# Kernel optimization log

Measured on AMD Instinct MI355X. Metric: run time of the kernel, lower is better.

The kernel has to match this reference:

```python
import jax, jax.numpy as jnp
import numpy as np

V = 32000; D = 128; L = 2048; B = 4
DI = 256; DS = 16; K = 4; H = 4; NM = 6; NA = 2; PAD = 0


def setup_inputs() -> dict:
    key = jax.random.key(0)
    ks = jax.random.split(key, 24)
    n = lambda i, shape, s: jax.random.normal(ks[i], shape, dtype=jnp.float32) * s
    inp = {}
    inp["input_ids"] = jax.random.randint(ks[0], (B, L), 0, V)
    inp["token_types"] = jax.random.randint(ks[1], (B, L), 0, 10)
    inp["timestamps"] = jax.random.uniform(ks[2], (B, L), dtype=jnp.float32)
    inp["emb"] = n(3, (V, D), 0.02).at[PAD].set(0.0)
    inp["type_emb"] = n(4, (10, D), 0.02)
    inp["te_freqs"] = n(5, (D // 2,), 0.1)
    inp["te_phases"] = jnp.zeros((D // 2,), jnp.float32)
    inp["te_w"] = n(6, (D, D), 0.05)
    inp["te_b"] = jnp.zeros((D,), jnp.float32)
    # Mamba blocks (stacked over NM)
    inp["m_norm_w"] = jnp.ones((NM, D), jnp.float32)
    inp["m_norm_b"] = jnp.zeros((NM, D), jnp.float32)
    inp["m_in_w"] = n(7, (NM, 2 * DI, D), 0.05)
    inp["m_conv_w"] = n(8, (NM, DI, 1, K), 0.2)   # depthwise, OIH with I=1
    inp["m_conv_b"] = jnp.zeros((NM, DI), jnp.float32)
    inp["m_dt_w"] = n(9, (NM, DI, DI), 0.05)
    inp["m_dt_b"] = jnp.zeros((NM, DI), jnp.float32)
    inp["m_B_w"] = n(10, (NM, DS, DI), 0.05)
    inp["m_C_w"] = n(11, (NM, DS, DI), 0.05)
    inp["m_D"] = jnp.ones((NM, DI), jnp.float32)
    inp["m_A_log"] = jnp.broadcast_to(jnp.log(jnp.arange(1, DS + 1, dtype=jnp.float32)), (NM, DI, DS)) + 0.0
    inp["m_out_w"] = n(12, (NM, D, DI), 0.05)
    # Attention blocks (stacked over NA)
    inp["a_ln1_w"] = jnp.ones((NA, D), jnp.float32)
    inp["a_ln1_b"] = jnp.zeros((NA, D), jnp.float32)
    inp["a_qkv_w"] = n(13, (NA, 3 * D, D), 0.05)
    inp["a_qkv_b"] = jnp.zeros((NA, 3 * D), jnp.float32)
    inp["a_out_w"] = n(14, (NA, D, D), 0.05)
    inp["a_out_b"] = jnp.zeros((NA, D), jnp.float32)
    inp["a_ln2_w"] = jnp.ones((NA, D), jnp.float32)
    inp["a_ln2_b"] = jnp.zeros((NA, D), jnp.float32)
    inp["a_f1_w"] = n(15, (NA, 4 * D, D), 0.05)
    inp["a_f1_b"] = jnp.zeros((NA, 4 * D), jnp.float32)
    inp["a_f2_w"] = n(16, (NA, D, 4 * D), 0.05)
    inp["a_f2_b"] = jnp.zeros((NA, D), jnp.float32)
    # Task head (n_tasks=1)
    inp["h_ln_w"] = jnp.ones((D,), jnp.float32)
    inp["h_ln_b"] = jnp.zeros((D,), jnp.float32)
    inp["h_w"] = n(17, (1, D), 0.05)
    inp["h_b"] = jnp.zeros((1,), jnp.float32)
    return inp


def _ln(x, w, b, eps=1e-5):
    mu = x.mean(-1, keepdims=True)
    var = ((x - mu) ** 2).mean(-1, keepdims=True)
    return (x - mu) * jax.lax.rsqrt(var + eps) * w + b


def _mamba(x, nw, nb, inw, cw, cb, dtw, dtb, bw, cpw, Dp, Alog, ow):
    res = x
    xn = _ln(x, nw, nb)
    xz = xn @ inw.T                              # [B,L,2*DI]
    xp, z = jnp.split(xz, 2, axis=-1)
    # causal depthwise conv: left-pad K-1, take first L outputs
    xc = jax.lax.conv_general_dilated(
        xp.transpose(0, 2, 1), cw, (1,), [(K - 1, 0)],
        feature_group_count=DI, dimension_numbers=("NCH", "OIH", "NCH"))
    xc = (xc + cb[None, :, None]).transpose(0, 2, 1)
    xc = jax.nn.silu(xc)
    dt = jax.nn.softplus(xc @ dtw.T + dtb)       # [B,L,DI]
    Bm = xc @ bw.T                               # [B,L,DS]
    Cm = xc @ cpw.T                              # [B,L,DS]
    A = -jnp.exp(Alog)                           # [DI,DS]

    def step(h, inp):
        dt_t, x_t, b_t, c_t = inp                # [B,DI],[B,DI],[B,DS],[B,DS]
        h = h * jnp.exp(A * dt_t[..., None]) + (x_t * dt_t)[..., None] * b_t[:, None, :]
        return h, (h * c_t[:, None, :]).sum(-1)

    xs = (jnp.moveaxis(dt, 1, 0), jnp.moveaxis(xc, 1, 0),
          jnp.moveaxis(Bm, 1, 0), jnp.moveaxis(Cm, 1, 0))
    h0 = jnp.zeros((x.shape[0], DI, DS), x.dtype)
    _, y = jax.lax.scan(step, h0, xs)            # y: [L,B,DI]
    y = jnp.moveaxis(y, 0, 1)
    y = y + xc * Dp
    y = y * jax.nn.silu(z)
    return res + y @ ow.T


def _attn(x, l1w, l1b, qkvw, qkvb, ow, ob, l2w, l2b, f1w, f1b, f2w, f2b):
    res = x
    xn = _ln(x, l1w, l1b)
    qkv = xn @ qkvw.T + qkvb
    q, k, v = jnp.split(qkv, 3, axis=-1)
    dh = D // H
    rs = lambda t: t.reshape(t.shape[0], t.shape[1], H, dh)
    q, k, v = rs(q), rs(k), rs(v)
    sc = jnp.einsum("bqhd,bkhd->bhqk", q, k) / jnp.sqrt(jnp.float32(dh))
    p = jax.nn.softmax(sc, axis=-1)
    o = jnp.einsum("bhqk,bkhd->bqhd", p, v).reshape(x.shape)
    x = res + o @ ow.T + ob
    ff = jax.nn.gelu(_ln(x, l2w, l2b) @ f1w.T + f1b, approximate=False) @ f2w.T + f2b
    return x + ff


def reference(input_ids, token_types, timestamps, emb, type_emb, te_freqs, te_phases, te_w, te_b,
              m_norm_w, m_norm_b, m_in_w, m_conv_w, m_conv_b, m_dt_w, m_dt_b, m_B_w, m_C_w,
              m_D, m_A_log, m_out_w,
              a_ln1_w, a_ln1_b, a_qkv_w, a_qkv_b, a_out_w, a_out_b, a_ln2_w, a_ln2_b,
              a_f1_w, a_f1_b, a_f2_w, a_f2_b, h_ln_w, h_ln_b, h_w, h_b):
    t = timestamps[..., None]
    enc = jnp.concatenate([jnp.sin(t * te_freqs + te_phases),
                           jnp.cos(t * te_freqs + te_phases)], axis=-1)
    x = emb[input_ids] + type_emb[token_types] + enc @ te_w.T + te_b
    attn_every = (NM + NA) // NA
    mi = 0; ai = 0
    for i in range(NM + NA):
        if (i + 1) % attn_every == 0:
            x = _attn(x, a_ln1_w[ai], a_ln1_b[ai], a_qkv_w[ai], a_qkv_b[ai],
                      a_out_w[ai], a_out_b[ai], a_ln2_w[ai], a_ln2_b[ai],
                      a_f1_w[ai], a_f1_b[ai], a_f2_w[ai], a_f2_b[ai])
            ai += 1
        else:
            x = _mamba(x, m_norm_w[mi], m_norm_b[mi], m_in_w[mi], m_conv_w[mi], m_conv_b[mi],
                       m_dt_w[mi], m_dt_b[mi], m_B_w[mi], m_C_w[mi], m_D[mi], m_A_log[mi], m_out_w[mi])
            mi += 1
    cls = x[:, 0, :]
    return (_ln(cls, h_ln_w, h_ln_b) @ h_w.T + h_b)[:, 0]
```

## Files before the change

kernel.cpp:

```cpp
#include <hip/hip_runtime.h>
#include <hip/hip_bf16.h>
#include <math.h>

constexpr int Ll = 2048, Bb = 4, DIi = 256, Hh = 4;
constexpr int TOK = Bb * Ll;
constexpr int NC = 128;
constexpr int CH = 16;
constexpr float LOG2E = 1.442695040888963f;

#define DEV __device__ __forceinline__

DEV float siluf(float v)     { return v / (1.f + expf(-v)); }
DEV float softplusf(float v) { return (v > 20.f) ? v : log1pf(expf(v)); }
DEV float geluf(float v)     { return 0.5f * v * (1.f + erff(v * 0.7071067811865476f)); }

#if defined(__has_builtin)
#if __has_builtin(__builtin_amdgcn_exp2f)
#define EXP2F __builtin_amdgcn_exp2f
#endif
#endif
#ifndef EXP2F
#define EXP2F exp2f
#endif

DEV short f2bf(float f) {
    union { float f; unsigned u; } a; a.f = f;
    unsigned r = (a.u + 0x7fffu + ((a.u >> 16) & 1u)) >> 16;
    return (short)r;
}

using bf16x8 = __attribute__((ext_vector_type(8))) short;
using f16x8  = __attribute__((ext_vector_type(8))) _Float16;
using f32x4  = __attribute__((ext_vector_type(4))) float;

__global__ __launch_bounds__(256) void wprep_kernel(
    const float* s0, const float* s1, const float* s2, const float* s3,
    const float* s4, const float* s5, const float* s6, const float* s7,
    const float* s8, const float* s9, _Float16* dst)
{
    constexpr int base[10] = {0, 16384, 409600, 802816, 827392, 851968,
                              1048576, 1146880, 1179648, 1310720};
    constexpr int nseg[10] = {16384, 393216, 393216, 24576, 24576, 196608,
                              98304, 32768, 131072, 131072};
    int seg = blockIdx.y;
    int t = blockIdx.x * 256 + threadIdx.x;
    if (t >= nseg[seg]) return;
    const float* src;
    switch (seg) {
        case 0: src = s0; break; case 1: src = s1; break;
        case 2: src = s2; break; case 3: src = s3; break;
        case 4: src = s4; break; case 5: src = s5; break;
        case 6: src = s6; break; case 7: src = s7; break;
        case 8: src = s8; break; default: src = s9; break;
    }
    dst[base[seg] + t] = (_Float16)src[t];
}

__global__ __launch_bounds__(256) void gather_enc_kernel(
    const int* __restrict__ ids, const int* __restrict__ tts,
    const float* __restrict__ ts, const float* __restrict__ emb,
    const float* __restrict__ temb, const float* __restrict__ freqs,
    const float* __restrict__ phases, float* __restrict__ x,
    float* __restrict__ enc)
{
    int tok = blockIdx.x * 2 + (threadIdx.x >> 7);
    int d = threadIdx.x & 127;
    float tval = ts[tok];
    int j = d & 63;
    float a = tval * freqs[j] + phases[j];
    enc[(size_t)tok * 128 + d] = (d < 64) ? sinf(a) : cosf(a);
    int id = ids[tok];
    int tt = tts[tok];
    x[(size_t)tok * 128 + d] = emb[(size_t)id * 128 + d] + temb[(size_t)tt * 128 + d];
}

template <int ACT, bool BIAS, bool ADD, bool LNA, int MODE>
__global__ __launch_bounds__(256) void gemm64_kernel(
    const float* __restrict__ A, const _Float16* __restrict__ W,
    const float* __restrict__ bias, float* __restrict__ C,
    const float* __restrict__ lnw, const float* __restrict__ lnb,
    const _Float16* __restrict__ Bw, const _Float16* __restrict__ Cw,
    float* __restrict__ bmo, float* __restrict__ cmo,
    short* __restrict__ kbf, short* __restrict__ vbf,
    int M, int N, int Kd, int lda, int ldc)
{
    constexpr int PADK = LNA ? 136 : 72;
    __shared__ _Float16 As[64][PADK];
    __shared__ _Float16 Ws[64][PADK];
    __shared__ float sMu[LNA ? 64 : 1];
    __shared__ float sRs[LNA ? 64 : 1];
    const int by = blockIdx.y;
    const bool isBC = (MODE == 1) && (by == (int)gridDim.y - 1);
    const int bm0 = blockIdx.x * 64, bn0 = by * 64;
    const int tid = threadIdx.x;
    const int w = tid >> 6, l = tid & 63;
    const int wr = w >> 1, wc = w & 1;
    const int fr = l & 15, fk = (l >> 4) * 8;
    const int srow = tid >> 2;
    f32x4 acc[2][2] = {};

    if (LNA) {
        const int kofs = (tid & 3) * 32;
        const float* ap = A + (size_t)(bm0 + srow) * lda + kofs;
        float av[32];
#pragma unroll
        for (int q = 0; q < 8; q++)
            *(float4*)(av + q * 4) = *(const float4*)(ap + q * 4);
        float s = 0.f, sq = 0.f;
#pragma unroll
        for (int q = 0; q < 32; q++) { s += av[q]; sq += av[q] * av[q]; }
        s  += __shfl_xor(s, 1);  s  += __shfl_xor(s, 2);
        sq += __shfl_xor(sq, 1); sq += __shfl_xor(sq, 2);
        if ((tid & 3) == 0) {
            float mu = s * (1.f / 128.f);
            float var = sq * (1.f / 128.f) - mu * mu;
            sMu[srow] = mu;
            sRs[srow] = rsqrtf(var + 1e-5f);
        }
        const _Float16* wp = W + (size_t)(bn0 + srow) * Kd + kofs;
        f16x8 wv0 = *(const f16x8*)wp,        wv1 = *(const f16x8*)(wp + 8);
        f16x8 wv2 = *(const f16x8*)(wp + 16), wv3 = *(const f16x8*)(wp + 24);
        __syncthreads();
        float mu = sMu[srow], rs = sRs[srow];
#pragma unroll
        for (int v = 0; v < 4; v++) {
            f16x8 a16;
#pragma unroll
            for (int j = 0; j < 8; j++) {
                float g = lnw[kofs + v * 8 + j];
                float bb = lnb[kofs + v * 8 + j];
                a16[j] = (_Float16)((av[v * 8 + j] - mu) * rs * g + bb);
            }
            *(f16x8*)&As[srow][kofs + v * 8] = a16;
        }
        *(f16x8*)&Ws[srow][kofs]      = wv0;
        *(f16x8*)&Ws[srow][kofs + 8]  = wv1;
        *(f16x8*)&Ws[srow][kofs + 16] = wv2;
        *(f16x8*)&Ws[srow][kofs + 24] = wv3;
        __syncthreads();
#pragma unroll
        for (int ks = 0; ks < 128; ks += 32) {
            f16x8 afr0 = *(const f16x8*)&As[wr * 32 + fr][ks + fk];
            f16x8 afr1 = *(const f16x8*)&As[wr * 32 + 16 + fr][ks + fk];
            f16x8 wfr0 = *(const f16x8*)&Ws[wc * 32 + fr][ks + fk];
            f16x8 wfr1 = *(const f16x8*)&Ws[wc * 32 + 16 + fr][ks + fk];
            acc[0][0] = __builtin_amdgcn_mfma_f32_16x16x32_f16(afr0, wfr0, acc[0][0], 0, 0, 0);
            acc[0][1] = __builtin_amdgcn_mfma_f32_16x16x32_f16(afr0, wfr1, acc[0][1], 0, 0, 0);
            acc[1][0] = __builtin_amdgcn_mfma_f32_16x16x32_f16(afr1, wfr0, acc[1][0], 0, 0, 0);
            acc[1][1] = __builtin_amdgcn_mfma_f32_16x16x32_f16(afr1, wfr1, acc[1][1], 0, 0, 0);
        }
    } else {
        const int skc = (tid & 3) * 16;
        for (int k0 = 0; k0 < Kd; k0 += 64) {
            const float* ap = A + (size_t)(bm0 + srow) * lda + k0 + skc;
            const _Float16* wp;
            if (isBC) {
                if (srow < 16)      wp = Bw + (size_t)srow * Kd + k0 + skc;
                else if (srow < 32) wp = Cw + (size_t)(srow - 16) * Kd + k0 + skc;
                else                wp = Bw + k0 + skc;
            } else {
                wp = W + (size_t)(bn0 + srow) * Kd + k0 + skc;
            }
            float af[16];
#pragma unroll
            for (int q = 0; q < 4; q++)
                *(float4*)(af + q * 4) = *(const float4*)(ap + q * 4);
            f16x8 wb0 = *(const f16x8*)wp;
            f16x8 wb1 = *(const f16x8*)(wp + 8);
            f16x8 ab0, ab1;
#pragma unroll
            for (int q = 0; q < 8; q++) {
                ab0[q] = (_Float16)af[q]; ab1[q] = (_Float16)af[q + 8];
            }
            __syncthreads();
            *(f16x8*)&As[srow][skc]     = ab0;
            *(f16x8*)&As[srow][skc + 8] = ab1;
            *(f16x8*)&Ws[srow][skc]     = wb0;
            *(f16x8*)&Ws[srow][skc + 8] = wb1;
            __syncthreads();
#pragma unroll
            for (int ks = 0; ks < 64; ks += 32) {
                f16x8 afr0 = *(const f16x8*)&As[wr * 32 + fr][ks + fk];
                f16x8 afr1 = *(const f16x8*)&As[wr * 32 + 16 + fr][ks + fk];
                f16x8 wfr0 = *(const f16x8*)&Ws[wc * 32 + fr][ks + fk];
                f16x8 wfr1 = *(const f16x8*)&Ws[wc * 32 + 16 + fr][ks + fk];
                acc[0][0] = __builtin_amdgcn_mfma_f32_16x16x32_f16(afr0, wfr0, acc[0][0], 0, 0, 0);
                acc[0][1] = __builtin_amdgcn_mfma_f32_16x16x32_f16(afr0, wfr1, acc[0][1], 0, 0, 0);
                acc[1][0] = __builtin_amdgcn_mfma_f32_16x16x32_f16(afr1, wfr0, acc[1][0], 0, 0, 0);
                acc[1][1] = __builtin_amdgcn_mfma_f32_16x16x32_f16(afr1, wfr1, acc[1][1], 0, 0, 0);
            }
        }
    }
#pragma unroll
    for (int ri = 0; ri < 2; ri++)
#pragma unroll
    for (int ci = 0; ci < 2; ci++) {
        const int lcol = wc * 32 + ci * 16 + fr;
        const int col = bn0 + lcol;
        const int row0 = bm0 + wr * 32 + ri * 16 + (l >> 4) * 4;
        if (isBC) {
            if (lcol < 32) {
                float* dst = (lcol < 16) ? bmo : cmo;
                const int cc = lcol & 15;
#pragma unroll
                for (int r = 0; r < 4; r++)
                    dst[(size_t)(row0 + r) * 16 + cc] = acc[ri][ci][r];
            }
        } else if (MODE == 2) {
            const float bv = bias[col];
            const int b = row0 >> 11, tl0 = row0 & 2047;
            if (col < 128) {
#pragma unroll
                for (int r = 0; r < 4; r++)
                    C[(size_t)(row0 + r) * 128 + col] = acc[ri][ci][r] + bv;
            } else if (col < 256) {
                const int hc = col - 128;
                short* kp = kbf + ((size_t)(b * 4 + (hc >> 5)) * 2048 + tl0) * 32 + (hc & 31);
#pragma unroll
                for (int r = 0; r < 4; r++)
                    kp[(size_t)r * 32] = f2bf(acc[ri][ci][r] + bv);
            } else {
                const int hc = col - 256;
                short4 vk;
#pragma unroll
                for (int r = 0; r < 4; r++)
                    ((short*)&vk)[r] = f2bf(acc[ri][ci][r] + bv);
                *(short4*)(vbf + ((size_t)(b * 4 + (hc >> 5)) * 32 + (hc & 31)) * 2048 + tl0) = vk;
            }
        } else {
            const float bv = BIAS ? bias[col] : 0.f;
#pragma unroll
            for (int r = 0; r < 4; r++) {
                float t = acc[ri][ci][r] + bv;
                if (ACT == 1) t = softplusf(t);
                if (ACT == 2) t = geluf(t);
                float* p = C + (size_t)(row0 + r) * ldc + col;
                if (ADD) t += *p;
                *p = t;
            }
        }
    }
}

__global__ __launch_bounds__(256) void conv_kernel(
    const float* __restrict__ xz, const float* __restrict__ cw,
    const float* __restrict__ cb, float* __restrict__ xc)
{
    int g = blockIdx.x * 256 + threadIdx.x;
    int c4 = g & 63;
    int t  = (g >> 6) & 2047;
    int b  = g >> 17;
    int c  = c4 * 4;
    float4 w0 = *(const float4*)(cw + (size_t)c * 4);
    float4 w1 = *(const float4*)(cw + (size_t)(c + 1) * 4);
    float4 w2 = *(const float4*)(cw + (size_t)(c + 2) * 4);
    float4 w3 = *(const float4*)(cw + (size_t)(c + 3) * 4);
    float4 bi = *(const float4*)(cb + c);
    float4 xk[4];
#pragma unroll
    for (int kk = 0; kk < 4; kk++) {
        int tt = t - 3 + kk;
        if (tt >= 0) xk[kk] = *(const float4*)(xz + ((size_t)b * 2048 + tt) * 512 + c);
        else xk[kk] = make_float4(0.f, 0.f, 0.f, 0.f);
    }
    float4 r;
    r.x = bi.x + xk[0].x * w0.x + xk[1].x * w0.y + xk[2].x * w0.z + xk[3].x * w0.w;
    r.y = bi.y + xk[0].y * w1.x + xk[1].y * w1.y + xk[2].y * w1.z + xk[3].y * w1.w;
    r.z = bi.z + xk[0].z * w2.x + xk[1].z * w2.y + xk[2].z * w2.z + xk[3].z * w2.w;
    r.w = bi.w + xk[0].w * w3.x + xk[1].w * w3.y + xk[2].w * w3.z + xk[3].w * w3.w;
    r.x = siluf(r.x); r.y = siluf(r.y); r.z = siluf(r.z); r.w = siluf(r.w);
    *(float4*)(xc + ((size_t)b * 2048 + t) * 256 + c) = r;
}

__global__ __launch_bounds__(256) void scan1_kernel(
    const float* __restrict__ dt, const float* __restrict__ xc,
    const float* __restrict__ bm, const float* __restrict__ Alog,
    float* __restrict__ F, float* __restrict__ sumdt)
{
    int c = threadIdx.x;
    int k = blockIdx.x & (NC - 1);
    int b = blockIdx.x / NC;
    __shared__ float sB[CH][16];
    int t0 = k * CH;
    if (threadIdx.x < CH * 4) {
        int r = threadIdx.x >> 2, c4 = (threadIdx.x & 3) << 2;
        *(float4*)&sB[r][c4] = *(const float4*)(bm + ((size_t)b * 2048 + t0 + r) * 16 + c4);
    }
    float A2[16];
#pragma unroll
    for (int s = 0; s < 16; s++) A2[s] = -expf(Alog[(size_t)c * 16 + s]) * LOG2E;
    __syncthreads();
    float h[16] = {};
    float sd = 0.f;
    size_t base = ((size_t)b * 2048 + t0) * 256 + c;
    for (int tt = 0; tt < CH; tt++) {
        float d  = dt[base + (size_t)tt * 256];
        float xv = xc[base + (size_t)tt * 256];
        sd += d;
        float xdt = xv * d;
#pragma unroll
        for (int s = 0; s < 16; s++) h[s] = h[s] * EXP2F(A2[s] * d) + xdt * sB[tt][s];
    }
    size_t fo = (((size_t)b * NC + k) * 256 + c) * 16;
#pragma unroll
    for (int s = 0; s < 16; s += 4) *(float4*)(F + fo + s) = make_float4(h[s], h[s+1], h[s+2], h[s+3]);
    sumdt[((size_t)b * NC + k) * 256 + c] = sd;
}

__global__ __launch_bounds__(256) void scan2_kernel(
    float* __restrict__ F, const float* __restrict__ sumdt,
    const float* __restrict__ Alog)
{
    int g = blockIdx.x * 256 + threadIdx.x;
    int s = g & 15, c = (g >> 4) & 255, b = g >> 12;
    float A2 = -expf(Alog[(size_t)c * 16 + s]) * LOG2E;
    float h = 0.f;
    for (int k = 0; k < NC; k++) {
        size_t o = (((size_t)b * NC + k) * 256 + c) * 16 + s;
        float tmp = F[o];
        F[o] = h;
        h = h * EXP2F(A2 * sumdt[((size_t)b * NC + k) * 256 + c]) + tmp;
    }
}

__global__ __launch_bounds__(256) void scan3_kernel(
    const float* __restrict__ dt, const float* __restrict__ xc,
    const float* __restrict__ bm, const float* __restrict__ cm,
    const float* __restrict__ xz, const float* __restrict__ Alog,
    const float* __restrict__ Dp, const float* __restrict__ Hs,
    float* __restrict__ y)
{
    int c = threadIdx.x;
    int k = blockIdx.x & (NC - 1);
    int b = blockIdx.x / NC;
    __shared__ float sB[CH][16], sC[CH][16];
    int t0 = k * CH;
    if (threadIdx.x < CH * 4) {
        int r = threadIdx.x >> 2, c4 = (threadIdx.x & 3) << 2;
        *(float4*)&sB[r][c4] = *(const float4*)(bm + ((size_t)b * 2048 + t0 + r) * 16 + c4);
        *(float4*)&sC[r][c4] = *(const float4*)(cm + ((size_t)b * 2048 + t0 + r) * 16 + c4);
    }
    float A2[16];
#pragma unroll
    for (int s = 0; s < 16; s++) A2[s] = -expf(Alog[(size_t)c * 16 + s]) * LOG2E;
    __syncthreads();
    float h[16];
    size_t ho = (((size_t)b * NC + k) * 256 + c) * 16;
#pragma unroll
    for (int s = 0; s < 16; s++) h[s] = Hs[ho + s];
    float Dv = Dp[c];
    size_t base  = ((size_t)b * 2048 + t0) * 256 + c;
    size_t zbase = ((size_t)b * 2048 + t0) * 512 + 256 + c;
    for (int tt = 0; tt < CH; tt++) {
        float d  = dt[base + (size_t)tt * 256];
        float xv = xc[base + (size_t)tt * 256];
        float xdt = xv * d;
        float yv = 0.f;
#pragma unroll
        for (int s = 0; s < 16; s++) {
            h[s] = h[s] * EXP2F(A2[s] * d) + xdt * sB[tt][s];
            yv += h[s] * sC[tt][s];
        }
        yv += xv * Dv;
        float zv = xz[zbase + (size_t)tt * 512];
        y[base + (size_t)tt * 256] = yv * siluf(zv);
    }
}

__global__ __launch_bounds__(256) void attn_part_kernel(
    const float* __restrict__ qbuf, const short* __restrict__ kbf,
    const short* __restrict__ vbf, float* __restrict__ pO, float* __restrict__ pml)
{
    __shared__ short Klds[2][64 * 32];
    __shared__ short Vlds[2][32 * 64];
    __shared__ short Pt[4][64][18];
    const int qt = blockIdx.x, b = blockIdx.z;
    const int h = blockIdx.y >> 2, sp = blockIdx.y & 3;
    const int tid = threadIdx.x;
    const int w = tid >> 6, l = tid & 63;
    const int q16 = l & 15, g = l >> 4;
    const float cQ = 0.25503634043f;

    const int qrow = qt * 64 + w * 16 + q16;
    const float* qp = qbuf + ((size_t)(b * 2048 + qrow)) * 128 + 32 * h + g * 8;
    bf16x8 qfrag;
    {
        float qf[8];
        *(float4*)qf       = *(const float4*)qp;
        *(float4*)(qf + 4) = *(const float4*)(qp + 4);
#pragma unroll
        for (int i = 0; i < 8; i++) qfrag[i] = f2bf(qf[i] * cQ);
    }
    const int bh = b * 4 + h;
    const short* kb = kbf + ((size_t)bh * 2048) * 32;
    const short* vb = vbf + ((size_t)bh * 32) * 2048;

    const int vrow = tid >> 3;
    const int vsw  = ((tid & 7) * 16) ^ ((vrow & 7) << 4);
    const int ts0 = sp * 8;

    bf16x8 kst, vst;
    auto ldregs = [&](int t) {
        kst = *(const bf16x8*)(kb + (size_t)t * 2048 + tid * 8);
        vst = *(const bf16x8*)(vb + (size_t)vrow * 2048 + t * 64 + (vsw >> 1));
    };
    auto dswrite = [&](int buf) {
        *(bf16x8*)&Klds[buf][tid * 8] = kst;
        *(bf16x8*)&Vlds[buf][tid * 8] = vst;
    };

    float m = -1e30f, lsum = 0.f;
    f32x4 O0 = {0.f, 0.f, 0.f, 0.f}, O1 = {0.f, 0.f, 0.f, 0.f};
    const f32x4 zf = {0.f, 0.f, 0.f, 0.f};

    auto step = [&](int buf) {
        bf16x8 kf[4];
#pragma unroll
        for (int kt = 0; kt < 4; kt++)
            kf[kt] = *(const bf16x8*)&Klds[buf][(kt * 16 + q16) * 32 + g * 8];
        f32x4 St[4];
#pragma unroll
        for (int kt = 0; kt < 4; kt++)
            St[kt] = __builtin_amdgcn_mfma_f32_16x16x32_bf16(kf[kt], qfrag, zf, 0, 0, 0);
        float pm = St[0][0];
#pragma unroll
        for (int kt = 0; kt < 4; kt++)
#pragma unroll
            for (int r = 0; r < 4; r++) pm = fmaxf(pm, St[kt][r]);
        pm = fmaxf(pm, __shfl_xor(pm, 16));
        pm = fmaxf(pm, __shfl_xor(pm, 32));
        float mn = fmaxf(m, pm);
        float rs = EXP2F(m - mn);
        float ps = 0.f;
#pragma unroll
        for (int kt = 0; kt < 4; kt++)
#pragma unroll
            for (int r = 0; r < 4; r++) {
                float p = EXP2F(St[kt][r] - mn);
                ps += p;
                Pt[w][kt * 16 + g * 4 + r][q16] = f2bf(p);
            }
        ps += __shfl_xor(ps, 16);
        ps += __shfl_xor(ps, 32);
        lsum = lsum * rs + ps;
        m = mn;
        O0 *= rs; O1 *= rs;
#pragma unroll
        for (int c = 0; c < 2; c++) {
            bf16x8 pb;
#pragma unroll
            for (int i = 0; i < 8; i++) pb[i] = Pt[w][c * 32 + g * 8 + i][q16];
#pragma unroll
            for (int hf = 0; hf < 2; hf++) {
                const int d = q16 + 16 * hf;
                bf16x8 vf = *(const bf16x8*)&Vlds[buf][d * 64 + ((c * 32 + g * 8) ^ ((d & 7) << 3))];
                if (hf == 0) O0 = __builtin_amdgcn_mfma_f32_16x16x32_bf16(vf, pb, O0, 0, 0, 0);
                else         O1 = __builtin_amdgcn_mfma_f32_16x16x32_bf16(vf, pb, O1, 0, 0, 0);
            }
        }
    };

    ldregs(ts0);
    dswrite(0);
    ldregs(ts0 + 1);
    int cur = 0;
    for (int i = 0; i < 8; i++) {
        __syncthreads();
        if (i + 1 < 8) {
            dswrite(cur ^ 1);
            if (i + 2 < 8) ldregs(ts0 + i + 2);
        }
        step(cur);
        cur ^= 1;
    }

    size_t po = (((size_t)(bh * 4 + sp)) * 2048 + qrow) * 32;
#pragma unroll
    for (int r = 0; r < 4; r++) {
        pO[po + g * 4 + r]      = O0[r];
        pO[po + 16 + g * 4 + r] = O1[r];
    }
    if (g == 0) {
        size_t mo = (((size_t)(bh * 4 + sp)) * 2048 + qrow) * 2;
        pml[mo]     = m;
        pml[mo + 1] = lsum;
    }
}

__global__ __launch_bounds__(256) void attn_comb_kernel(
    const float* __restrict__ pO, const float* __restrict__ pml,
    float* __restrict__ aout)
{
    int gid = blockIdx.x * 256 + threadIdx.x;
    int d = gid & 31, q = (gid >> 5) & 2047, bh = gid >> 16;
    float m[4], lv[4], M = -1e30f;
#pragma unroll
    for (int s = 0; s < 4; s++) {
        size_t mo = (((size_t)(bh * 4 + s)) * 2048 + q) * 2;
        m[s] = pml[mo]; lv[s] = pml[mo + 1];
        M = fmaxf(M, m[s]);
    }
    float L = 0.f, o = 0.f;
#pragma unroll
    for (int s = 0; s < 4; s++) {
        float wgt = EXP2F(m[s] - M);
        L += lv[s] * wgt;
        o += pO[(((size_t)(bh * 4 + s)) * 2048 + q) * 32 + d] * wgt;
    }
    int b = bh >> 2, h = bh & 3;
    aout[((size_t)(b * 2048 + q)) * 128 + h * 32 + d] = o / L;
}

__global__ __launch_bounds__(128) void head_kernel(
    const float* __restrict__ x, const float* __restrict__ w,
    const float* __restrict__ bsp, const float* __restrict__ hw,
    const float* __restrict__ hb, float* __restrict__ out)
{
    int bb = blockIdx.x;
    int d = threadIdx.x;
    int wid = d >> 6, lane = d & 63;
    float v = x[(size_t)bb * 2048 * 128 + d];
    float s = v, sq = v * v;
#pragma unroll
    for (int o = 32; o > 0; o >>= 1) { s += __shfl_xor(s, o); sq += __shfl_xor(sq, o); }
    __shared__ float red[4];
    if (lane == 0) { red[wid] = s; red[2 + wid] = sq; }
    __syncthreads();
    s = red[0] + red[1]; sq = red[2] + red[3];
    float mu = s * (1.f / 128.f);
    float var = sq * (1.f / 128.f) - mu * mu;
    float xn = (v - mu) * rsqrtf(var + 1e-5f) * w[d] + bsp[d];
    float pr = xn * hw[d];
#pragma unroll
    for (int o = 32; o > 0; o >>= 1) pr += __shfl_xor(pr, o);
    __syncthreads();
    if (lane == 0) red[wid] = pr;
    __syncthreads();
    if (d == 0) out[bb] = red[0] + red[1] + hb[0];
}

constexpr size_t OFF_X  = 0;
constexpr size_t OFF_XZ = (size_t)1 << 20;
constexpr size_t OFF_XC = (size_t)5 << 20;
constexpr size_t OFF_DT = (size_t)7 << 20;
constexpr size_t OFF_Y  = (size_t)9 << 20;
constexpr size_t OFF_BM = (size_t)11 << 20;
constexpr size_t OFF_CM = OFF_BM + 131072;
constexpr size_t OFF_SD = OFF_CM + 131072;
constexpr size_t OFF_ST = OFF_SD + 131072;
constexpr size_t OFF_F  = OFF_ST + 16384;
constexpr size_t OFF_WF = OFF_F + ((size_t)2 << 20);
constexpr size_t WS_FLOATS = OFF_WF + 720896;

extern "C" void kernel_launch(void* const* d_in, const int* in_sizes, int n_in,
                              void* d_out, int out_size, void* d_ws, size_t ws_size,
                              hipStream_t stream)
{
    const int*   ids   = (const int*)d_in[0];
    const int*   tts   = (const int*)d_in[1];
    const float* tstmp = (const float*)d_in[2];
    const float* emb   = (const float*)d_in[3];
    const float* temb  = (const float*)d_in[4];
    const float* tef   = (const float*)d_in[5];
    const float* tep   = (const float*)d_in[6];
    const float* tew   = (const float*)d_in[7];
    const float* tebi  = (const float*)d_in[8];
    const float* mnw   = (const float*)d_in[9];
    const float* mnb   = (const float*)d_in[10];
    const float* minw  = (const float*)d_in[11];
    const float* mcwp  = (const float*)d_in[12];
    const float* mcb   = (const float*)d_in[13];
    const float* mdtw  = (const float*)d_in[14];
    const float* mdtb  = (const float*)d_in[15];
    const float* mbw   = (const float*)d_in[16];
    const float* mcw2  = (const float*)d_in[17];
    const float* mD    = (const float*)d_in[18];
    const float* mAl   = (const float*)d_in[19];
    const float* mow   = (const float*)d_in[20];
    const float* al1w  = (const float*)d_in[21];
    const float* al1b  = (const float*)d_in[22];
    const float* aqkvw = (const float*)d_in[23];
    const float* aqkvb = (const float*)d_in[24];
    const float* aow   = (const float*)d_in[25];
    const float* aob   = (const float*)d_in[26];
    const float* al2w  = (const float*)d_in[27];
    const float* al2b  = (const float*)d_in[28];
    const float* af1w  = (const float*)d_in[29];
    const float* af1b  = (const float*)d_in[30];
    const float* af2w  = (const float*)d_in[31];
    const float* af2b  = (const float*)d_in[32];
    const float* hlnw  = (const float*)d_in[33];
    const float* hlnb  = (const float*)d_in[34];
    const float* hw    = (const float*)d_in[35];
    const float* hb    = (const float*)d_in[36];
    float* out = (float*)d_out;
    float* wsf = (float*)d_ws;
    if (ws_size < WS_FLOATS * sizeof(float)) return;

    float* x    = wsf + OFF_X;
    float* xz   = wsf + OFF_XZ;
    float* xc   = wsf + OFF_XC;
    float* dtb  = wsf + OFF_DT;
    float* yb   = wsf + OFF_Y;
    float* bm   = wsf + OFF_BM;
    float* cm   = wsf + OFF_CM;
    float* sdb  = wsf + OFF_SD;
    float* Fb   = wsf + OFF_F;
    float* ff   = xz;
    float* aout = yb;
    float* qbuf = xc;
    float* pO   = xz;
    float* pml  = dtb;
    float* encb = Fb;
    short* kbf  = (short*)(wsf + OFF_F);
    short* vbf  = (short*)(wsf + OFF_F + ((size_t)1 << 20));
    _Float16* wf16 = (_Float16*)(wsf + OFF_WF);

    const _Float16* tew16   = wf16;
    const _Float16* minw16  = wf16 + 16384;
    const _Float16* mdtw16  = wf16 + 409600;
    const _Float16* mbw16   = wf16 + 802816;
    const _Float16* mcw216  = wf16 + 827392;
    const _Float16* mow16   = wf16 + 851968;
    const _Float16* aqkvw16 = wf16 + 1048576;
    const _Float16* aow16   = wf16 + 1146880;
    const _Float16* af1w16  = wf16 + 1179648;
    const _Float16* af2w16  = wf16 + 1310720;

    wprep_kernel<<<dim3(1536, 10), 256, 0, stream>>>(
        tew, minw, mdtw, mbw, mcw2, mow, aqkvw, aow, af1w, af2w, wf16);

    gather_enc_kernel<<<TOK / 2, 256, 0, stream>>>(ids, tts, tstmp, emb, temb, tef, tep, x, encb);
    gemm64_kernel<0, true, true, false, 0><<<dim3(128, 2), 256, 0, stream>>>(
        encb, tew16, tebi, x, nullptr, nullptr, nullptr, nullptr,
        nullptr, nullptr, nullptr, nullptr, TOK, 128, 128, 128, 128);

    int mi = 0, ai = 0;
    for (int i = 0; i < 8; i++) {
        if ((i + 1) % 4 == 0) {
            gemm64_kernel<0, true, false, true, 2><<<dim3(128, 6), 256, 0, stream>>>(
                x, aqkvw16 + (size_t)ai * 49152, aqkvb + ai * 384, qbuf,
                al1w + ai * 128, al1b + ai * 128, nullptr, nullptr,
                nullptr, nullptr, kbf, vbf, TOK, 384, 128, 128, 128);
            attn_part_kernel<<<dim3(32, 16, Bb), 256, 0, stream>>>(qbuf, kbf, vbf, pO, pml);
            attn_comb_kernel<<<4096, 256, 0, stream>>>(pO, pml, aout);
            gemm64_kernel<0, true, true, false, 0><<<dim3(128, 2), 256, 0, stream>>>(
                aout, aow16 + (size_t)ai * 16384, aob + ai * 128, x,
                nullptr, nullptr, nullptr, nullptr,
                nullptr, nullptr, nullptr, nullptr, TOK, 128, 128, 128, 128);
            gemm64_kernel<2, true, false, true, 0><<<dim3(128, 8), 256, 0, stream>>>(
                x, af1w16 + (size_t)ai * 65536, af1b + ai * 512, ff,
                al2w + ai * 128, al2b + ai * 128, nullptr, nullptr,
                nullptr, nullptr, nullptr, nullptr, TOK, 512, 128, 128, 512);
            gemm64_kernel<0, true, true, false, 0><<<dim3(128, 2), 256, 0, stream>>>(
                ff, af2w16 + (size_t)ai * 65536, af2b + ai * 128, x,
                nullptr, nullptr, nullptr, nullptr,
                nullptr, nullptr, nullptr, nullptr, TOK, 128, 512, 512, 128);
            ai++;
        } else {
            const float* Al = mAl + (size_t)mi * DIi * 16;
            gemm64_kernel<0, false, false, true, 0><<<dim3(128, 8), 256, 0, stream>>>(
                x, minw16 + (size_t)mi * 65536, nullptr, xz,
                mnw + mi * 128, mnb + mi * 128, nullptr, nullptr,
                nullptr, nullptr, nullptr, nullptr, TOK, 512, 128, 128, 512);
            conv_kernel<<<2048, 256, 0, stream>>>(xz, mcwp + (size_t)mi * DIi * 4, mcb + mi * DIi, xc);
            gemm64_kernel<1, true, false, false, 1><<<dim3(128, 5), 256, 0, stream>>>(
                xc, mdtw16 + (size_t)mi * 65536, mdtb + mi * 256, dtb,
                nullptr, nullptr,
                mbw16 + (size_t)mi * 4096, mcw216 + (size_t)mi * 4096,
                bm, cm, nullptr, nullptr, TOK, 256, 256, 256, 256);
            scan1_kernel<<<Bb * NC, 256, 0, stream>>>(dtb, xc, bm, Al, Fb, sdb);
            scan2_kernel<<<64, 256, 0, stream>>>(Fb, sdb, Al);
            scan3_kernel<<<Bb * NC, 256, 0, stream>>>(dtb, xc, bm, cm, xz, Al, mD + mi * 256, Fb, yb);
            gemm64_kernel<0, false, true, false, 0><<<dim3(128, 2), 256, 0, stream>>>(
                yb, mow16 + (size_t)mi * 32768, nullptr, x,
                nullptr, nullptr, nullptr, nullptr,
                nullptr, nullptr, nullptr, nullptr, TOK, 128, 256, 256, 128);
            mi++;
        }
    }
    head_kernel<<<Bb, 128, 0, stream>>>(x, hlnw, hlnb, hw, hb, out);
}
```

Measured before the change: 714.1 us.

## Fuse depthwise conv into dt GEMM and attention combine into out-proj GEMM

The causal depthwise conv + SiLU is now computed inside the dt/B/C GEMM's A-tile load, with blocks in the first column tile also writing xc for the scan, so the standalone conv kernel is dropped. The attention split-softmax combine is folded into the out-projection GEMM's A-load (new MODE 3), removing attn_comb_kernel and the aout round-trip. scan1 is also restructured to load dt and x*dt for the chunk first and then run the recurrence per state, which exposes more independent work. The cost is redundant conv and combine work across column-tile blocks and extra global loads per A tile.

```diff
diff --git a/kernel.cpp b/kernel.cpp
--- a/kernel.cpp
+++ b/kernel.cpp
@@ -82,6 +82,9 @@
     const _Float16* __restrict__ Bw, const _Float16* __restrict__ Cw,
     float* __restrict__ bmo, float* __restrict__ cmo,
     short* __restrict__ kbf, short* __restrict__ vbf,
+    const float* __restrict__ cvw, const float* __restrict__ cvb,
+    float* __restrict__ xco,
+    const float* __restrict__ pOin, const float* __restrict__ pmlin,
     int M, int N, int Kd, int lda, int ldc)
 {
     constexpr int PADK = LNA ? 136 : 72;
@@ -89,6 +92,8 @@
     __shared__ _Float16 Ws[64][PADK];
     __shared__ float sMu[LNA ? 64 : 1];
     __shared__ float sRs[LNA ? 64 : 1];
+    __shared__ float cwS[(MODE == 1) ? 256 : 1][4];
+    __shared__ float cbS[(MODE == 1) ? 256 : 1];
     const int by = blockIdx.y;
     const bool isBC = (MODE == 1) && (by == (int)gridDim.y - 1);
     const int bm0 = blockIdx.x * 64, bn0 = by * 64;
@@ -99,6 +104,12 @@
     const int srow = tid >> 2;
     f32x4 acc[2][2] = {};
 
+    if (MODE == 1) {
+        *(float4*)&cwS[tid][0] = *(const float4*)(cvw + (size_t)tid * 4);
+        cbS[tid] = cvb[tid];
+        __syncthreads();
+    }
+
     if (LNA) {
         const int kofs = (tid & 3) * 32;
         const float* ap = A + (size_t)(bm0 + srow) * lda + kofs;
@@ -152,7 +163,75 @@
     } else {
         const int skc = (tid & 3) * 16;
         for (int k0 = 0; k0 < Kd; k0 += 64) {
-            const float* ap = A + (size_t)(bm0 + srow) * lda + k0 + skc;
+            float af[16];
+            if (MODE == 1) {
+                const int tglob = bm0 + srow;
+                const int bb = tglob >> 11, tl = tglob & 2047;
+                const size_t rowb = (size_t)bb * 2048;
+#pragma unroll
+                for (int q4 = 0; q4 < 4; q4++) {
+                    const int cb0 = k0 + skc + q4 * 4;
+                    float4 xr[4];
+#pragma unroll
+                    for (int kk = 0; kk < 4; kk++) {
+                        int tt = tl - 3 + kk;
+                        xr[kk] = (tt >= 0) ? *(const float4*)(A + (rowb + tt) * 512 + cb0)
+                                           : make_float4(0.f, 0.f, 0.f, 0.f);
+                    }
+#pragma unroll
+                    for (int j = 0; j < 4; j++) {
+                        const int col = cb0 + j;
+                        float a0 = cbS[col]
+                            + ((const float*)&xr[0])[j] * cwS[col][0]
+                            + ((const float*)&xr[1])[j] * cwS[col][1]
+                            + ((const float*)&xr[2])[j] * cwS[col][2]
+                            + ((const float*)&xr[3])[j] * cwS[col][3];
+                        af[q4 * 4 + j] = siluf(a0);
+                    }
+                }
+                if (by == 0) {
+#pragma unroll
+                    for (int q4 = 0; q4 < 4; q4++)
+                        *(float4*)(xco + (size_t)tglob * 256 + k0 + skc + q4 * 4) =
+                            make_float4(af[q4*4], af[q4*4+1], af[q4*4+2], af[q4*4+3]);
+                }
+            } else if (MODE == 3) {
+                const int tglob = bm0 + srow;
+                const int bb = tglob >> 11, q = tglob & 2047;
+                const int base = k0 + skc;
+                const int h = base >> 5, d0 = base & 31;
+                const int bh = bb * 4 + h;
+                float m[4], lv[4], M = -1e30f;
+#pragma unroll
+                for (int s = 0; s < 4; s++) {
+                    size_t mo = (((size_t)(bh * 4 + s)) * 2048 + q) * 2;
+                    m[s] = pmlin[mo]; lv[s] = pmlin[mo + 1];
+                    M = fmaxf(M, m[s]);
+                }
+                float L = 0.f, wgt[4];
+#pragma unroll
+                for (int s = 0; s < 4; s++) { wgt[s] = EXP2F(m[s] - M); L += lv[s] * wgt[s]; }
+                float inv = 1.f / L;
+#pragma unroll
+                for (int j = 0; j < 16; j++) af[j] = 0.f;
+#pragma unroll
+                for (int s = 0; s < 4; s++) {
+                    const float* pp = pOin + (((size_t)(bh * 4 + s)) * 2048 + q) * 32 + d0;
+#pragma unroll
+                    for (int q4 = 0; q4 < 4; q4++) {
+                        float4 v = *(const float4*)(pp + q4 * 4);
+                        af[q4*4+0] += v.x * wgt[s]; af[q4*4+1] += v.y * wgt[s];
+                        af[q4*4+2] += v.z * wgt[s]; af[q4*4+3] += v.w * wgt[s];
+                    }
+                }
+#pragma unroll
+                for (int j = 0; j < 16; j++) af[j] *= inv;
+            } else {
+                const float* ap = A + (size_t)(bm0 + srow) * lda + k0 + skc;
+#pragma unroll
+                for (int q = 0; q < 4; q++)
+                    *(float4*)(af + q * 4) = *(const float4*)(ap + q * 4);
+            }
             const _Float16* wp;
             if (isBC) {
                 if (srow < 16)      wp = Bw + (size_t)srow * Kd + k0 + skc;
@@ -161,10 +240,6 @@
             } else {
                 wp = W + (size_t)(bn0 + srow) * Kd + k0 + skc;
             }
-            float af[16];
-#pragma unroll
-            for (int q = 0; q < 4; q++)
-                *(float4*)(af + q * 4) = *(const float4*)(ap + q * 4);
             f16x8 wb0 = *(const f16x8*)wp;
             f16x8 wb1 = *(const f16x8*)(wp + 8);
             f16x8 ab0, ab1;
@@ -242,36 +317,6 @@
     }
 }
 
-__global__ __launch_bounds__(256) void conv_kernel(
-    const float* __restrict__ xz, const float* __restrict__ cw,
-    const float* __restrict__ cb, float* __restrict__ xc)
-{
-    int g = blockIdx.x * 256 + threadIdx.x;
-    int c4 = g & 63;
-    int t  = (g >> 6) & 2047;
-    int b  = g >> 17;
-    int c  = c4 * 4;
-    float4 w0 = *(const float4*)(cw + (size_t)c * 4);
-    float4 w1 = *(const float4*)(cw + (size_t)(c + 1) * 4);
-    float4 w2 = *(const float4*)(cw + (size_t)(c + 2) * 4);
-    float4 w3 = *(const float4*)(cw + (size_t)(c + 3) * 4);
-    float4 bi = *(const float4*)(cb + c);
-    float4 xk[4];
-#pragma unroll
-    for (int kk = 0; kk < 4; kk++) {
-        int tt = t - 3 + kk;
-        if (tt >= 0) xk[kk] = *(const float4*)(xz + ((size_t)b * 2048 + tt) * 512 + c);
-        else xk[kk] = make_float4(0.f, 0.f, 0.f, 0.f);
-    }
-    float4 r;
-    r.x = bi.x + xk[0].x * w0.x + xk[1].x * w0.y + xk[2].x * w0.z + xk[3].x * w0.w;
-    r.y = bi.y + xk[0].y * w1.x + xk[1].y * w1.y + xk[2].y * w1.z + xk[3].y * w1.w;
-    r.z = bi.z + xk[0].z * w2.x + xk[1].z * w2.y + xk[2].z * w2.z + xk[3].z * w2.w;
-    r.w = bi.w + xk[0].w * w3.x + xk[1].w * w3.y + xk[2].w * w3.z + xk[3].w * w3.w;
-    r.x = siluf(r.x); r.y = siluf(r.y); r.z = siluf(r.z); r.w = siluf(r.w);
-    *(float4*)(xc + ((size_t)b * 2048 + t) * 256 + c) = r;
-}
-
 __global__ __launch_bounds__(256) void scan1_kernel(
     const float* __restrict__ dt, const float* __restrict__ xc,
     const float* __restrict__ bm, const float* __restrict__ Alog,
@@ -290,16 +335,24 @@
 #pragma unroll
     for (int s = 0; s < 16; s++) A2[s] = -expf(Alog[(size_t)c * 16 + s]) * LOG2E;
     __syncthreads();
-    float h[16] = {};
+    size_t base = ((size_t)b * 2048 + t0) * 256 + c;
+    float dts[CH], xds[CH];
     float sd = 0.f;
-    size_t base = ((size_t)b * 2048 + t0) * 256 + c;
+#pragma unroll
     for (int tt = 0; tt < CH; tt++) {
         float d  = dt[base + (size_t)tt * 256];
         float xv = xc[base + (size_t)tt * 256];
-        sd += d;
-        float xdt = xv * d;
-#pragma unroll
-        for (int s = 0; s < 16; s++) h[s] = h[s] * EXP2F(A2[s] * d) + xdt * sB[tt][s];
+        dts[tt] = d; sd += d; xds[tt] = xv * d;
+    }
+    float h[16];
+#pragma unroll
+    for (int s = 0; s < 16; s++) {
+        float A2s = A2[s];
+        float hh = 0.f;
+#pragma unroll
+        for (int tt = 0; tt < CH; tt++)
+            hh = hh * EXP2F(A2s * dts[tt]) + xds[tt] * sB[tt][s];
+        h[s] = hh;
     }
     size_t fo = (((size_t)b * NC + k) * 256 + c) * 16;
 #pragma unroll
@@ -485,30 +538,6 @@
         pml[mo]     = m;
         pml[mo + 1] = lsum;
     }
-}
-
-__global__ __launch_bounds__(256) void attn_comb_kernel(
-    const float* __restrict__ pO, const float* __restrict__ pml,
-    float* __restrict__ aout)
-{
-    int gid = blockIdx.x * 256 + threadIdx.x;
-    int d = gid & 31, q = (gid >> 5) & 2047, bh = gid >> 16;
-    float m[4], lv[4], M = -1e30f;
-#pragma unroll
-    for (int s = 0; s < 4; s++) {
-        size_t mo = (((size_t)(bh * 4 + s)) * 2048 + q) * 2;
-        m[s] = pml[mo]; lv[s] = pml[mo + 1];
-        M = fmaxf(M, m[s]);
-    }
-    float L = 0.f, o = 0.f;
-#pragma unroll
-    for (int s = 0; s < 4; s++) {
-        float wgt = EXP2F(m[s] - M);
-        L += lv[s] * wgt;
-        o += pO[(((size_t)(bh * 4 + s)) * 2048 + q) * 32 + d] * wgt;
-    }
-    int b = bh >> 2, h = bh & 3;
-    aout[((size_t)(b * 2048 + q)) * 128 + h * 32 + d] = o / L;
 }
 
 __global__ __launch_bounds__(128) void head_kernel(
@@ -607,7 +636,6 @@
     float* sdb  = wsf + OFF_SD;
     float* Fb   = wsf + OFF_F;
     float* ff   = xz;
-    float* aout = yb;
     float* qbuf = xc;
     float* pO   = xz;
     float* pml  = dtb;
@@ -633,7 +661,8 @@
     gather_enc_kernel<<<TOK / 2, 256, 0, stream>>>(ids, tts, tstmp, emb, temb, tef, tep, x, encb);
     gemm64_kernel<0, true, true, false, 0><<<dim3(128, 2), 256, 0, stream>>>(
         encb, tew16, tebi, x, nullptr, nullptr, nullptr, nullptr,
-        nullptr, nullptr, nullptr, nullptr, TOK, 128, 128, 128, 128);
+        nullptr, nullptr, nullptr, nullptr,
+        nullptr, nullptr, nullptr, nullptr, nullptr, TOK, 128, 128, 128, 128);
 
     int mi = 0, ai = 0;
     for (int i = 0; i < 8; i++) {
@@ -641,41 +670,47 @@
             gemm64_kernel<0, true, false, true, 2><<<dim3(128, 6), 256, 0, stream>>>(
                 x, aqkvw16 + (size_t)ai * 49152, aqkvb + ai * 384, qbuf,
                 al1w + ai * 128, al1b + ai * 128, nullptr, nullptr,
-                nullptr, nullptr, kbf, vbf, TOK, 384, 128, 128, 128);
+                nullptr, nullptr, kbf, vbf,
+                nullptr, nullptr, nullptr, nullptr, nullptr, TOK, 384, 128, 128, 128);
             attn_part_kernel<<<dim3(32, 16, Bb), 256, 0, stream>>>(qbuf, kbf, vbf, pO, pml);
-            attn_comb_kernel<<<4096, 256, 0, stream>>>(pO, pml, aout);
-            gemm64_kernel<0, true, true, false, 0><<<dim3(128, 2), 256, 0, stream>>>(
-                aout, aow16 + (size_t)ai * 16384, aob + ai * 128, x,
+            gemm64_kernel<0, true, true, false, 3><<<dim3(128, 2), 256, 0, stream>>>(
+                nullptr, aow16 + (size_t)ai * 16384, aob + ai * 128, x,
                 nullptr, nullptr, nullptr, nullptr,
-                nullptr, nullptr, nullptr, nullptr, TOK, 128, 128, 128, 128);
+                nullptr, nullptr, nullptr, nullptr,
+                nullptr, nullptr, nullptr, pO, pml, TOK, 128, 128, 128, 128);
             gemm64_kernel<2, true, false, true, 0><<<dim3(128, 8), 256, 0, stream>>>(
                 x, af1w16 + (size_t)ai * 65536, af1b + ai * 512, ff,
                 al2w + ai * 128, al2b + ai * 128, nullptr, nullptr,
-                nullptr, nullptr, nullptr, nullptr, TOK, 512, 128, 128, 512);
+                nullptr, nullptr, nullptr, nullptr,
+                nullptr, nullptr, nullptr, nullptr, nullptr, TOK, 512, 128, 128, 512);
             gemm64_kernel<0, true, true, false, 0><<<dim3(128, 2), 256, 0, stream>>>(
                 ff, af2w16 + (size_t)ai * 65536, af2b + ai * 128, x,
                 nullptr, nullptr, nullptr, nullptr,
-                nullptr, nullptr, nullptr, nullptr, TOK, 128, 512, 512, 128);
+                nullptr, nullptr, nullptr, nullptr,
+                nullptr, nullptr, nullptr, nullptr, nullptr, TOK, 128, 512, 512, 128);
             ai++;
         } else {
             const float* Al = mAl + (size_t)mi * DIi * 16;
             gemm64_kernel<0, false, false, true, 0><<<dim3(128, 8), 256, 0, stream>>>(
                 x, minw16 + (size_t)mi * 65536, nullptr, xz,
                 mnw + mi * 128, mnb + mi * 128, nullptr, nullptr,
-                nullptr, nullptr, nullptr, nullptr, TOK, 512, 128, 128, 512);
-            conv_kernel<<<2048, 256, 0, stream>>>(xz, mcwp + (size_t)mi * DIi * 4, mcb + mi * DIi, xc);
+                nullptr, nullptr, nullptr, nullptr,
+                nullptr, nullptr, nullptr, nullptr, nullptr, TOK, 512, 128, 128, 512);
             gemm64_kernel<1, true, false, false, 1><<<dim3(128, 5), 256, 0, stream>>>(
-                xc, mdtw16 + (size_t)mi * 65536, mdtb + mi * 256, dtb,
+                xz, mdtw16 + (size_t)mi * 65536, mdtb + mi * 256, dtb,
                 nullptr, nullptr,
                 mbw16 + (size_t)mi * 4096, mcw216 + (size_t)mi * 4096,
-                bm, cm, nullptr, nullptr, TOK, 256, 256, 256, 256);
+                bm, cm, nullptr, nullptr,
+                mcwp + (size_t)mi * DIi * 4, mcb + mi * DIi, xc,
+                nullptr, nullptr, TOK, 256, 256, 512, 256);
             scan1_kernel<<<Bb * NC, 256, 0, stream>>>(dtb, xc, bm, Al, Fb, sdb);
             scan2_kernel<<<64, 256, 0, stream>>>(Fb, sdb, Al);
             scan3_kernel<<<Bb * NC, 256, 0, stream>>>(dtb, xc, bm, cm, xz, Al, mD + mi * 256, Fb, yb);
             gemm64_kernel<0, false, true, false, 0><<<dim3(128, 2), 256, 0, stream>>>(
                 yb, mow16 + (size_t)mi * 32768, nullptr, x,
                 nullptr, nullptr, nullptr, nullptr,
-                nullptr, nullptr, nullptr, nullptr, TOK, 128, 256, 256, 128);
+                nullptr, nullptr, nullptr, nullptr,
+                nullptr, nullptr, nullptr, nullptr, nullptr, TOK, 128, 256, 256, 128);
             mi++;
         }
     }
```

New measurement: 746.4 us. 4.5% more time.
